# Kernel optimization log

Hardware: AMD Instinct MI355X
Metric: run time of the kernel (lower is better)

The kernel has to match this reference:

```python
import jax, jax.numpy as jnp
import numpy as np

N = 100000   # nodes
E = 1600000  # edges (avg degree 16)
D = 128      # input_dim == hidden_dim
H = 128
L = 3        # n_layers
G = 512      # num graphs in batch
LATENT = 64
BN_EPS = 1e-5
SLOPE = 0.2  # LeakyReLU negative slope


def setup_inputs() -> dict:
    key = jax.random.key(0)
    ks = jax.random.split(key, 12)
    s = 1.0 / np.sqrt(H)
    return {
        "x": jax.random.normal(ks[0], (N, D), jnp.float32),
        "edge_index": jax.random.randint(ks[1], (2, E), 0, N, dtype=jnp.int32),
        "batch": jnp.sort(jax.random.randint(ks[2], (N,), 0, G, dtype=jnp.int32)),
        "W1": jax.random.normal(ks[3], (L, D, H), jnp.float32) * s,
        "b1": jax.random.normal(ks[4], (L, H), jnp.float32) * 0.01,
        "g1": jnp.ones((L, H), jnp.float32),
        "beta1": jnp.zeros((L, H), jnp.float32),
        "rm1": jnp.zeros((L, H), jnp.float32),
        "rv1": jnp.ones((L, H), jnp.float32),
        "W2": jax.random.normal(ks[5], (L, H, H), jnp.float32) * s,
        "b2": jax.random.normal(ks[6], (L, H), jnp.float32) * 0.01,
        "bn_g": jnp.ones((H,), jnp.float32),
        "bn_b": jnp.zeros((H,), jnp.float32),
        "bn_rm": jnp.zeros((H,), jnp.float32),
        "bn_rv": jnp.ones((H,), jnp.float32),
        "fcW": jax.random.normal(ks[7], (H, LATENT), jnp.float32) * s,
        "fcb": jax.random.normal(ks[8], (LATENT,), jnp.float32) * 0.01,
    }


def _bn_eval(t, g, b, rm, rv):
    # BatchNorm1d in eval mode: normalize by running stats
    return g * (t - rm) * jax.lax.rsqrt(rv + BN_EPS) + b


def reference(x, edge_index, batch, W1, b1, g1, beta1, rm1, rv1, W2, b2,
              bn_g, bn_b, bn_rm, bn_rv, fcW, fcb):
    src, dst = edge_index[0], edge_index[1]
    h = x
    for i in range(L):
        # GINConv (eps=0): h_i <- MLP(h_i + sum_{j->i} h_j)
        agg = jax.ops.segment_sum(h[src], dst, num_segments=N)
        t = (h + agg) @ W1[i] + b1[i]
        t = jax.nn.leaky_relu(t, SLOPE)
        t = _bn_eval(t, g1[i], beta1[i], rm1[i], rv1[i])
        t = t @ W2[i] + b2[i]
        h = jax.nn.leaky_relu(t, SLOPE)
        # dropout: identity in eval mode
    # global add pool by graph id -> [G, H]
    pooled = jax.ops.segment_sum(h, batch, num_segments=G)
    pooled = _bn_eval(pooled, bn_g, bn_b, bn_rm, bn_rv)
    return pooled @ fcW + fcb
```

## Files before the change

kernel.cpp:

```cpp
#include <hip/hip_runtime.h>

#define NN 100000
#define EE 1600000
#define DD 128
#define HH 128
#define LL 3
#define GG 512
#define LATENT 64
#define BN_EPS 1e-5f
#define SLOPE 0.2f
#define NB_SCAN 391
#define ASTR 136

typedef __attribute__((ext_vector_type(8))) short short8;
typedef __attribute__((ext_vector_type(4))) float floatx4;

__device__ __forceinline__ float leaky(float t) { return t > 0.f ? t : SLOPE * t; }

__device__ __forceinline__ unsigned short f2bf(float x) {
    union { float f; unsigned int u; } v; v.f = x;
    unsigned int r = v.u + 0x7fffu + ((v.u >> 16) & 1u);
    return (unsigned short)(r >> 16);
}
__device__ __forceinline__ float bf_lo(unsigned int p) {
    union { unsigned int u; float f; } v; v.u = p << 16; return v.f;
}
__device__ __forceinline__ float bf_hi(unsigned int p) {
    union { unsigned int u; float f; } v; v.u = p & 0xffff0000u; return v.f;
}


__global__ void hist_kernel(const int* __restrict__ dst, int* __restrict__ deg, int* __restrict__ rank) {
    int e = blockIdx.x * blockDim.x + threadIdx.x;
    if (e < EE) rank[e] = atomicAdd(&deg[dst[e]], 1);
}

__global__ __launch_bounds__(256) void scan1(const int* __restrict__ deg, int* __restrict__ bsum) {
    __shared__ int lds[256];
    int n = blockIdx.x * 256 + threadIdx.x;
    lds[threadIdx.x] = (n < NN) ? deg[n] : 0;
    __syncthreads();
    for (int off = 128; off > 0; off >>= 1) {
        if (threadIdx.x < off) lds[threadIdx.x] += lds[threadIdx.x + off];
        __syncthreads();
    }
    if (threadIdx.x == 0) bsum[blockIdx.x] = lds[0];
}

__global__ __launch_bounds__(512) void scan2(int* bsum, int* row_ptr) {
    __shared__ int lds[512];
    int tid = threadIdx.x;
    int v = (tid < NB_SCAN) ? bsum[tid] : 0;
    lds[tid] = v;
    __syncthreads();
    for (int off = 1; off < 512; off <<= 1) {
        int t = (tid >= off) ? lds[tid - off] : 0;
        __syncthreads();
        lds[tid] += t;
        __syncthreads();
    }
    int inc = lds[tid];
    if (tid < NB_SCAN) bsum[tid] = inc - v;
    if (tid == NB_SCAN - 1) row_ptr[NN] = inc;
}

__global__ __launch_bounds__(256) void scan3(const int* __restrict__ deg, const int* __restrict__ bsumEx,
                                             int* __restrict__ row_ptr) {
    __shared__ int lds[256];
    int tid = threadIdx.x;
    int n = blockIdx.x * 256 + tid;
    int v = (n < NN) ? deg[n] : 0;
    lds[tid] = v;
    __syncthreads();
    for (int off = 1; off < 256; off <<= 1) {
        int t = (tid >= off) ? lds[tid - off] : 0;
        __syncthreads();
        lds[tid] += t;
        __syncthreads();
    }
    int ex = lds[tid] - v;
    if (n < NN) row_ptr[n] = bsumEx[blockIdx.x] + ex;
}

__global__ void fill2(const int* __restrict__ src, const int* __restrict__ dst,
                      const int* __restrict__ rank, const int* __restrict__ row_ptr,
                      int* __restrict__ col) {
    int e = blockIdx.x * blockDim.x + threadIdx.x;
    if (e < EE) col[row_ptr[dst[e]] + rank[e]] = src[e];
}

__global__ void gstart_kernel(const int* __restrict__ batch, int* __restrict__ gstart) {
    int n = blockIdx.x * blockDim.x + threadIdx.x;
    if (n >= NN) return;
    int b = batch[n];
    int pb = (n == 0) ? -1 : batch[n - 1];
    for (int g = pb + 1; g <= b; ++g) gstart[g] = n;
    if (n == NN - 1) {
        for (int g = b + 1; g <= GG; ++g) gstart[g] = NN;
    }
}


__global__ __launch_bounds__(256) void cvtX(const float2* __restrict__ x2, unsigned int* __restrict__ hx) {
    int i = blockIdx.x * 256 + threadIdx.x;
    if (i >= NN * 64) return;
    float2 v = x2[i];
    hx[i] = (unsigned int)f2bf(v.x) | ((unsigned int)f2bf(v.y) << 16);
}

__global__ __launch_bounds__(256) void cvtWall(const float* __restrict__ W1,
                                               const float* __restrict__ W2,
                                               uint4* __restrict__ Wf) {
    int t = blockIdx.x * 256 + threadIdx.x;
    if (t >= 6 * 2048) return;
    int mat = t >> 11;
    int idx = t & 2047;
    const float* W = ((mat & 1) ? W2 : W1) + (size_t)(mat >> 1) * 128 * 128;
    int lane = idx & 63;
    int tn = (idx >> 6) & 7;
    int kk = idx >> 9;
    int n = tn * 16 + (lane & 15);
    int kb = kk * 32 + (lane >> 4) * 8;
    unsigned int p[4];
#pragma unroll
    for (int jj = 0; jj < 4; ++jj) {
        unsigned short lo = f2bf(W[(kb + 2 * jj) * 128 + n]);
        unsigned short hi = f2bf(W[(kb + 2 * jj + 1) * 128 + n]);
        p[jj] = (unsigned int)lo | ((unsigned int)hi << 16);
    }
    Wf[t] = make_uint4(p[0], p[1], p[2], p[3]);
}

__global__ __launch_bounds__(256) void agg_bf16w8(const unsigned int* __restrict__ h,
                                                  const int* __restrict__ row_ptr,
                                                  const int* __restrict__ col,
                                                  unsigned int* __restrict__ u) {
    int node = blockIdx.x * 4 + (threadIdx.x >> 6);
    int lane = threadIdx.x & 63;
    if (node >= NN) return;
    const int grp = lane >> 3;
    const int sub = lane & 7;
    const uint4* hv = (const uint4*)h;

    float a[16] = {};
    if (grp == 0) {
        uint4 v0 = hv[(size_t)node * 16 + sub];
        uint4 v1 = hv[(size_t)node * 16 + 8 + sub];
        a[0] += bf_lo(v0.x); a[1] += bf_hi(v0.x);
        a[2] += bf_lo(v0.y); a[3] += bf_hi(v0.y);
        a[4] += bf_lo(v0.z); a[5] += bf_hi(v0.z);
        a[6] += bf_lo(v0.w); a[7] += bf_hi(v0.w);
        a[8] += bf_lo(v1.x); a[9] += bf_hi(v1.x);
        a[10] += bf_lo(v1.y); a[11] += bf_hi(v1.y);
        a[12] += bf_lo(v1.z); a[13] += bf_hi(v1.z);
        a[14] += bf_lo(v1.w); a[15] += bf_hi(v1.w);
    }
    int s = row_ptr[node], e = row_ptr[node + 1];
    for (int j = s + grp; j < e; j += 8) {
        int c = col[j];
        uint4 v0 = hv[(size_t)c * 16 + sub];
        uint4 v1 = hv[(size_t)c * 16 + 8 + sub];
        a[0] += bf_lo(v0.x); a[1] += bf_hi(v0.x);
        a[2] += bf_lo(v0.y); a[3] += bf_hi(v0.y);
        a[4] += bf_lo(v0.z); a[5] += bf_hi(v0.z);
        a[6] += bf_lo(v0.w); a[7] += bf_hi(v0.w);
        a[8] += bf_lo(v1.x); a[9] += bf_hi(v1.x);
        a[10] += bf_lo(v1.y); a[11] += bf_hi(v1.y);
        a[12] += bf_lo(v1.z); a[13] += bf_hi(v1.z);
        a[14] += bf_lo(v1.w); a[15] += bf_hi(v1.w);
    }
#pragma unroll
    for (int t = 0; t < 16; ++t) {
        a[t] += __shfl_xor(a[t], 8);
        a[t] += __shfl_xor(a[t], 16);
        a[t] += __shfl_xor(a[t], 32);
    }
    if (grp == 0) {
        uint4 o0, o1;
        o0.x = (unsigned int)f2bf(a[0]) | ((unsigned int)f2bf(a[1]) << 16);
        o0.y = (unsigned int)f2bf(a[2]) | ((unsigned int)f2bf(a[3]) << 16);
        o0.z = (unsigned int)f2bf(a[4]) | ((unsigned int)f2bf(a[5]) << 16);
        o0.w = (unsigned int)f2bf(a[6]) | ((unsigned int)f2bf(a[7]) << 16);
        o1.x = (unsigned int)f2bf(a[8]) | ((unsigned int)f2bf(a[9]) << 16);
        o1.y = (unsigned int)f2bf(a[10]) | ((unsigned int)f2bf(a[11]) << 16);
        o1.z = (unsigned int)f2bf(a[12]) | ((unsigned int)f2bf(a[13]) << 16);
        o1.w = (unsigned int)f2bf(a[14]) | ((unsigned int)f2bf(a[15]) << 16);
        ((uint4*)u)[(size_t)node * 16 + sub] = o0;
        ((uint4*)u)[(size_t)node * 16 + 8 + sub] = o1;
    }
}

__global__ __launch_bounds__(256) void mlp_fused(const unsigned short* __restrict__ A,
                                                 const uint4* __restrict__ W1f,
                                                 const uint4* __restrict__ W2f,
                                                 const float* __restrict__ b1,
                                                 const float* __restrict__ g,
                                                 const float* __restrict__ beta,
                                                 const float* __restrict__ rm,
                                                 const float* __restrict__ rv,
                                                 const float* __restrict__ b2,
                                                 unsigned short* __restrict__ Out) {
    __shared__ unsigned short aL[128 * ASTR];
    __shared__ unsigned short mL[4][32 * ASTR];
    const int tid = threadIdx.x;
    const int rb = blockIdx.x * 128;

    const uint4* Ag = (const uint4*)(A + (size_t)rb * 128);
#pragma unroll
    for (int it = 0; it < 8; ++it) {
        int idx = it * 256 + tid;
        int r = idx >> 4, c = idx & 15;
        uint4 v = make_uint4(0u, 0u, 0u, 0u);
        if (rb + r < NN) v = Ag[idx];
        *(uint4*)&aL[r * ASTR + c * 8] = v;
    }
    __syncthreads();

    const int wid = tid >> 6, lane = tid & 63;
    const int ml = lane & 15, q = lane >> 4;
    const int m0 = wid * 32;

    floatx4 acc[2][8] = {};
#pragma unroll
    for (int kk = 0; kk < 4; ++kk) {
        short8 af[2];
#pragma unroll
        for (int t = 0; t < 2; ++t)
            af[t] = *(const short8*)&aL[(m0 + t * 16 + ml) * ASTR + kk * 32 + q * 8];
#pragma unroll
        for (int tn = 0; tn < 8; ++tn) {
            uint4 bq = W1f[(kk * 8 + tn) * 64 + lane];
            short8 bf = *(short8*)&bq;
            acc[0][tn] = __builtin_amdgcn_mfma_f32_16x16x32_bf16(af[0], bf, acc[0][tn], 0, 0, 0);
            acc[1][tn] = __builtin_amdgcn_mfma_f32_16x16x32_bf16(af[1], bf, acc[1][tn], 0, 0, 0);
        }
    }

#pragma unroll
    for (int tn = 0; tn < 8; ++tn) {
        int c = tn * 16 + ml;
        float s = g[c] * rsqrtf(rv[c] + BN_EPS);
        float sh = beta[c] - s * rm[c];
        float bv = b1[c];
#pragma unroll
        for (int t = 0; t < 2; ++t)
#pragma unroll
            for (int r = 0; r < 4; ++r) {
                float val = leaky(acc[t][tn][r] + bv);
                val = s * val + sh;
                mL[wid][(t * 16 + q * 4 + r) * ASTR + c] = f2bf(val);
            }
    }
    __syncthreads();

    floatx4 acc2[2][8] = {};
#pragma unroll
    for (int kk = 0; kk < 4; ++kk) {
        short8 af[2];
#pragma unroll
        for (int t = 0; t < 2; ++t)
            af[t] = *(const short8*)&mL[wid][(t * 16 + ml) * ASTR + kk * 32 + q * 8];
#pragma unroll
        for (int tn = 0; tn < 8; ++tn) {
            uint4 bq = W2f[(kk * 8 + tn) * 64 + lane];
            short8 bf = *(short8*)&bq;
            acc2[0][tn] = __builtin_amdgcn_mfma_f32_16x16x32_bf16(af[0], bf, acc2[0][tn], 0, 0, 0);
            acc2[1][tn] = __builtin_amdgcn_mfma_f32_16x16x32_bf16(af[1], bf, acc2[1][tn], 0, 0, 0);
        }
    }

#pragma unroll
    for (int tn = 0; tn < 8; ++tn) {
        int c = tn * 16 + ml;
        float bv = b2[c];
#pragma unroll
        for (int t = 0; t < 2; ++t)
#pragma unroll
            for (int r = 0; r < 4; ++r) {
                int row = rb + m0 + t * 16 + q * 4 + r;
                if (row < NN)
                    Out[(size_t)row * 128 + c] = f2bf(leaky(acc2[t][tn][r] + bv));
            }
    }
}

__global__ __launch_bounds__(256) void pool_bf16(const unsigned int* __restrict__ h,
                                                 const int* __restrict__ gstart,
                                                 const float* __restrict__ bng,
                                                 const float* __restrict__ bnb,
                                                 const float* __restrict__ bnrm,
                                                 const float* __restrict__ bnrv,
                                                 float* __restrict__ pooled) {
    __shared__ float lds[4][128];
    int g = blockIdx.x;
    int wid = threadIdx.x >> 6, lane = threadIdx.x & 63;
    int s = gstart[g], e = gstart[g + 1];
    float ax = 0.f, ay = 0.f;
    for (int n = s + wid; n < e; n += 4) {
        unsigned int v = h[(size_t)n * 64 + lane];
        ax += bf_lo(v);
        ay += bf_hi(v);
    }
    lds[wid][lane * 2] = ax;
    lds[wid][lane * 2 + 1] = ay;
    __syncthreads();
    if (wid == 0) {
#pragma unroll
        for (int t = 0; t < 2; ++t) {
            int c = lane * 2 + t;
            float acc = lds[0][c] + lds[1][c] + lds[2][c] + lds[3][c];
            pooled[g * 128 + c] = bng[c] * (acc - bnrm[c]) * rsqrtf(bnrv[c] + BN_EPS) + bnb[c];
        }
    }
}

__global__ __launch_bounds__(64) void final_kernel(const float* __restrict__ pooled,
                                                   const float* __restrict__ fcW,
                                                   const float* __restrict__ fcb,
                                                   float* __restrict__ out) {
    int g = blockIdx.x;
    int l = threadIdx.x;
    float acc = fcb[l];
#pragma unroll 8
    for (int c = 0; c < HH; ++c) acc += pooled[g * 128 + c] * fcW[c * LATENT + l];
    out[g * LATENT + l] = acc;
}

extern "C" void kernel_launch(void* const* d_in, const int* in_sizes, int n_in,
                              void* d_out, int out_size, void* d_ws, size_t ws_size,
                              hipStream_t stream) {
    const float* x = (const float*)d_in[0];
    const int* ei = (const int*)d_in[1];
    const int* batch = (const int*)d_in[2];
    const float* W1 = (const float*)d_in[3];
    const float* b1 = (const float*)d_in[4];
    const float* g1 = (const float*)d_in[5];
    const float* beta1 = (const float*)d_in[6];
    const float* rm1 = (const float*)d_in[7];
    const float* rv1 = (const float*)d_in[8];
    const float* W2 = (const float*)d_in[9];
    const float* b2 = (const float*)d_in[10];
    const float* bn_g = (const float*)d_in[11];
    const float* bn_b = (const float*)d_in[12];
    const float* bn_rm = (const float*)d_in[13];
    const float* bn_rv = (const float*)d_in[14];
    const float* fcW = (const float*)d_in[15];
    const float* fcb = (const float*)d_in[16];
    float* out = (float*)d_out;

    const int* src = ei;
    const int* dst = ei + EE;

    char* w = (char*)d_ws;
    size_t off = 0;
    auto alloc = [&](size_t bytes) -> char* {
        char* p = w + off;
        off += (bytes + 1023) & ~(size_t)1023;
        return p;
    };
    unsigned int* hx = (unsigned int*)alloc(4 * (size_t)NN * 64);
    unsigned int* ubuf = (unsigned int*)alloc(4 * (size_t)NN * 64);
    unsigned int* hbuf = (unsigned int*)alloc(4 * (size_t)NN * 64);
    uint4* Wf = (uint4*)alloc(16 * (size_t)6 * 2048);
    int* deg = (int*)alloc(4 * (size_t)NN);
    int* row_ptr = (int*)alloc(4 * (size_t)(NN + 1));
    int* rank = (int*)alloc(4 * (size_t)EE);
    int* col = (int*)alloc(4 * (size_t)EE);
    int* bsum = (int*)alloc(4 * 512);
    int* gstart = (int*)alloc(4 * (GG + 1));
    float* pooled = (float*)alloc(sizeof(float) * GG * 128);
    (void)ws_size; (void)in_sizes; (void)n_in; (void)out_size;

    hipMemsetAsync(deg, 0, 4 * (size_t)NN, stream);
    hist_kernel<<<(EE + 255) / 256, 256, 0, stream>>>(dst, deg, rank);
    scan1<<<NB_SCAN, 256, 0, stream>>>(deg, bsum);
    scan2<<<1, 512, 0, stream>>>(bsum, row_ptr);
    scan3<<<NB_SCAN, 256, 0, stream>>>(deg, bsum, row_ptr);
    fill2<<<(EE + 255) / 256, 256, 0, stream>>>(src, dst, rank, row_ptr, col);
    gstart_kernel<<<(NN + 255) / 256, 256, 0, stream>>>(batch, gstart);

    cvtX<<<(NN * 64 + 255) / 256, 256, 0, stream>>>((const float2*)x, hx);
    cvtWall<<<48, 256, 0, stream>>>(W1, W2, Wf);

    const int gblocks = (NN + 127) / 128;
    const unsigned int* hcur = hx;
    for (int i = 0; i < LL; ++i) {
        agg_bf16w8<<<(NN + 3) / 4, 256, 0, stream>>>(hcur, row_ptr, col, ubuf);
        mlp_fused<<<gblocks, 256, 0, stream>>>((const unsigned short*)ubuf,
                                               Wf + (size_t)(2 * i) * 2048,
                                               Wf + (size_t)(2 * i + 1) * 2048,
                                               b1 + i * HH, g1 + i * HH, beta1 + i * HH,
                                               rm1 + i * HH, rv1 + i * HH, b2 + i * HH,
                                               (unsigned short*)hbuf);
        hcur = hbuf;
    }
    pool_bf16<<<GG, 256, 0, stream>>>(hbuf, gstart, bn_g, bn_b, bn_rm, bn_rv, pooled);
    final_kernel<<<GG, 64, 0, stream>>>(pooled, fcW, fcb, out);
}
```

Baseline: 563.2 us.

## Privatize degree histogram per XCD, merge prep kernels, pack aggregation into float2

The degree histogram now keeps a private copy per XCD, picked by reading the hardware XCC id, so atomics stay in each die's local L2 rather than bouncing across dies. A combine pass then computes per-XCD offsets, and fill writes CSR columns from those offsets. The gstart, weight-conversion and x-conversion kernels are merged into one launch to cut launch overhead. Aggregation accumulates in float2 vectors to allow packed adds. The cost is an 8x larger degree buffer plus its memset, and the code depends on reading an undocumented hardware register.

After: 564.6 us. Within noise of the previous version (+0.3%).

```diff
diff --git a/kernel.cpp b/kernel.cpp
--- a/kernel.cpp
+++ b/kernel.cpp
@@ -9,11 +9,13 @@
 #define LATENT 64
 #define BN_EPS 1e-5f
 #define SLOPE 0.2f
+#define ASTR 136
 #define NB_SCAN 391
-#define ASTR 136
+#define NXCD 8
 
 typedef __attribute__((ext_vector_type(8))) short short8;
 typedef __attribute__((ext_vector_type(4))) float floatx4;
+typedef __attribute__((ext_vector_type(2))) float floatx2;
 
 __device__ __forceinline__ float leaky(float t) { return t > 0.f ? t : SLOPE * t; }
 
@@ -28,17 +30,44 @@
 __device__ __forceinline__ float bf_hi(unsigned int p) {
     union { unsigned int u; float f; } v; v.u = p & 0xffff0000u; return v.f;
 }
-
-
-__global__ void hist_kernel(const int* __restrict__ dst, int* __restrict__ deg, int* __restrict__ rank) {
+__device__ __forceinline__ floatx2 up2(unsigned int p) {
+    union { unsigned int u; float f; } lo, hi;
+    lo.u = p << 16; hi.u = p & 0xffff0000u;
+    floatx2 r; r.x = lo.f; r.y = hi.f; return r;
+}
+
+__device__ __forceinline__ int xcc_id() {
+    int x;
+    asm volatile("s_getreg_b32 %0, hwreg(HW_REG_XCC_ID)" : "=s"(x));
+    return x & (NXCD - 1);
+}
+
+
+__global__ void hist_x(const int* __restrict__ dst, int* __restrict__ deg8, int* __restrict__ rank) {
+    int x = xcc_id();
     int e = blockIdx.x * blockDim.x + threadIdx.x;
-    if (e < EE) rank[e] = atomicAdd(&deg[dst[e]], 1);
-}
-
-__global__ __launch_bounds__(256) void scan1(const int* __restrict__ deg, int* __restrict__ bsum) {
+    if (e < EE) {
+        int d = dst[e];
+        int r = atomicAdd(&deg8[x * NN + d], 1);
+        rank[e] = (x << 24) | r;
+    }
+}
+
+__global__ __launch_bounds__(256) void combine(int* __restrict__ deg8, int* __restrict__ deg,
+                                               int* __restrict__ bsum) {
     __shared__ int lds[256];
     int n = blockIdx.x * 256 + threadIdx.x;
-    lds[threadIdx.x] = (n < NN) ? deg[n] : 0;
+    int tot = 0;
+    if (n < NN) {
+#pragma unroll
+        for (int x = 0; x < NXCD; ++x) {
+            int c = deg8[x * NN + n];
+            deg8[x * NN + n] = tot;
+            tot += c;
+        }
+        deg[n] = tot;
+    }
+    lds[threadIdx.x] = tot;
     __syncthreads();
     for (int off = 128; off > 0; off >>= 1) {
         if (threadIdx.x < off) lds[threadIdx.x] += lds[threadIdx.x + off];
@@ -82,54 +111,60 @@
     if (n < NN) row_ptr[n] = bsumEx[blockIdx.x] + ex;
 }
 
-__global__ void fill2(const int* __restrict__ src, const int* __restrict__ dst,
+__global__ void fill3(const int* __restrict__ src, const int* __restrict__ dst,
                       const int* __restrict__ rank, const int* __restrict__ row_ptr,
-                      int* __restrict__ col) {
+                      const int* __restrict__ xoff, int* __restrict__ col) {
     int e = blockIdx.x * blockDim.x + threadIdx.x;
-    if (e < EE) col[row_ptr[dst[e]] + rank[e]] = src[e];
-}
-
-__global__ void gstart_kernel(const int* __restrict__ batch, int* __restrict__ gstart) {
-    int n = blockIdx.x * blockDim.x + threadIdx.x;
-    if (n >= NN) return;
-    int b = batch[n];
-    int pb = (n == 0) ? -1 : batch[n - 1];
-    for (int g = pb + 1; g <= b; ++g) gstart[g] = n;
-    if (n == NN - 1) {
-        for (int g = b + 1; g <= GG; ++g) gstart[g] = NN;
-    }
-}
-
-
-__global__ __launch_bounds__(256) void cvtX(const float2* __restrict__ x2, unsigned int* __restrict__ hx) {
-    int i = blockIdx.x * 256 + threadIdx.x;
-    if (i >= NN * 64) return;
-    float2 v = x2[i];
-    hx[i] = (unsigned int)f2bf(v.x) | ((unsigned int)f2bf(v.y) << 16);
-}
-
-__global__ __launch_bounds__(256) void cvtWall(const float* __restrict__ W1,
-                                               const float* __restrict__ W2,
-                                               uint4* __restrict__ Wf) {
-    int t = blockIdx.x * 256 + threadIdx.x;
-    if (t >= 6 * 2048) return;
-    int mat = t >> 11;
-    int idx = t & 2047;
-    const float* W = ((mat & 1) ? W2 : W1) + (size_t)(mat >> 1) * 128 * 128;
-    int lane = idx & 63;
-    int tn = (idx >> 6) & 7;
-    int kk = idx >> 9;
-    int n = tn * 16 + (lane & 15);
-    int kb = kk * 32 + (lane >> 4) * 8;
-    unsigned int p[4];
-#pragma unroll
-    for (int jj = 0; jj < 4; ++jj) {
-        unsigned short lo = f2bf(W[(kb + 2 * jj) * 128 + n]);
-        unsigned short hi = f2bf(W[(kb + 2 * jj + 1) * 128 + n]);
-        p[jj] = (unsigned int)lo | ((unsigned int)hi << 16);
-    }
-    Wf[t] = make_uint4(p[0], p[1], p[2], p[3]);
-}
+    if (e < EE) {
+        int d = dst[e];
+        int rk = rank[e];
+        int x = rk >> 24;
+        int lr = rk & 0xffffff;
+        col[row_ptr[d] + xoff[x * NN + d] + lr] = src[e];
+    }
+}
+
+#define PREP_GS 391
+#define PREP_W  (PREP_GS + 48)
+__global__ __launch_bounds__(256) void prep_kernel(const int* __restrict__ batch, int* __restrict__ gstart,
+                                                   const float* __restrict__ W1, const float* __restrict__ W2,
+                                                   uint4* __restrict__ Wf,
+                                                   const float2* __restrict__ x2, unsigned int* __restrict__ hx) {
+    int b = blockIdx.x;
+    if (b < PREP_GS) {
+        int n = b * 256 + threadIdx.x;
+        if (n >= NN) return;
+        int bb = batch[n];
+        int pb = (n == 0) ? -1 : batch[n - 1];
+        for (int g = pb + 1; g <= bb; ++g) gstart[g] = n;
+        if (n == NN - 1)
+            for (int g = bb + 1; g <= GG; ++g) gstart[g] = NN;
+    } else if (b < PREP_W) {
+        int t = (b - PREP_GS) * 256 + threadIdx.x;
+        int mat = t >> 11;
+        int idx = t & 2047;
+        const float* W = ((mat & 1) ? W2 : W1) + (size_t)(mat >> 1) * 128 * 128;
+        int lane = idx & 63;
+        int tn = (idx >> 6) & 7;
+        int kk = idx >> 9;
+        int n = tn * 16 + (lane & 15);
+        int kb = kk * 32 + (lane >> 4) * 8;
+        unsigned int p[4];
+#pragma unroll
+        for (int jj = 0; jj < 4; ++jj) {
+            unsigned short lo = f2bf(W[(kb + 2 * jj) * 128 + n]);
+            unsigned short hi = f2bf(W[(kb + 2 * jj + 1) * 128 + n]);
+            p[jj] = (unsigned int)lo | ((unsigned int)hi << 16);
+        }
+        Wf[t] = make_uint4(p[0], p[1], p[2], p[3]);
+    } else {
+        int i = (b - PREP_W) * 256 + threadIdx.x;
+        if (i >= NN * 64) return;
+        float2 v = x2[i];
+        hx[i] = (unsigned int)f2bf(v.x) | ((unsigned int)f2bf(v.y) << 16);
+    }
+}
+#define PREP_BLOCKS (PREP_W + (NN * 64 + 255) / 256)
 
 __global__ __launch_bounds__(256) void agg_bf16w8(const unsigned int* __restrict__ h,
                                                   const int* __restrict__ row_ptr,
@@ -142,49 +177,43 @@
     const int sub = lane & 7;
     const uint4* hv = (const uint4*)h;
 
-    float a[16] = {};
+    floatx2 a[8];
+#pragma unroll
+    for (int t = 0; t < 8; ++t) { a[t].x = 0.f; a[t].y = 0.f; }
+
     if (grp == 0) {
         uint4 v0 = hv[(size_t)node * 16 + sub];
         uint4 v1 = hv[(size_t)node * 16 + 8 + sub];
-        a[0] += bf_lo(v0.x); a[1] += bf_hi(v0.x);
-        a[2] += bf_lo(v0.y); a[3] += bf_hi(v0.y);
-        a[4] += bf_lo(v0.z); a[5] += bf_hi(v0.z);
-        a[6] += bf_lo(v0.w); a[7] += bf_hi(v0.w);
-        a[8] += bf_lo(v1.x); a[9] += bf_hi(v1.x);
-        a[10] += bf_lo(v1.y); a[11] += bf_hi(v1.y);
-        a[12] += bf_lo(v1.z); a[13] += bf_hi(v1.z);
-        a[14] += bf_lo(v1.w); a[15] += bf_hi(v1.w);
+        a[0] += up2(v0.x); a[1] += up2(v0.y); a[2] += up2(v0.z); a[3] += up2(v0.w);
+        a[4] += up2(v1.x); a[5] += up2(v1.y); a[6] += up2(v1.z); a[7] += up2(v1.w);
     }
     int s = row_ptr[node], e = row_ptr[node + 1];
     for (int j = s + grp; j < e; j += 8) {
         int c = col[j];
         uint4 v0 = hv[(size_t)c * 16 + sub];
         uint4 v1 = hv[(size_t)c * 16 + 8 + sub];
-        a[0] += bf_lo(v0.x); a[1] += bf_hi(v0.x);
-        a[2] += bf_lo(v0.y); a[3] += bf_hi(v0.y);
-        a[4] += bf_lo(v0.z); a[5] += bf_hi(v0.z);
-        a[6] += bf_lo(v0.w); a[7] += bf_hi(v0.w);
-        a[8] += bf_lo(v1.x); a[9] += bf_hi(v1.x);
-        a[10] += bf_lo(v1.y); a[11] += bf_hi(v1.y);
-        a[12] += bf_lo(v1.z); a[13] += bf_hi(v1.z);
-        a[14] += bf_lo(v1.w); a[15] += bf_hi(v1.w);
-    }
-#pragma unroll
-    for (int t = 0; t < 16; ++t) {
-        a[t] += __shfl_xor(a[t], 8);
-        a[t] += __shfl_xor(a[t], 16);
-        a[t] += __shfl_xor(a[t], 32);
+        a[0] += up2(v0.x); a[1] += up2(v0.y); a[2] += up2(v0.z); a[3] += up2(v0.w);
+        a[4] += up2(v1.x); a[5] += up2(v1.y); a[6] += up2(v1.z); a[7] += up2(v1.w);
+    }
+#pragma unroll
+    for (int t = 0; t < 8; ++t) {
+        a[t].x += __shfl_xor(a[t].x, 8);
+        a[t].y += __shfl_xor(a[t].y, 8);
+        a[t].x += __shfl_xor(a[t].x, 16);
+        a[t].y += __shfl_xor(a[t].y, 16);
+        a[t].x += __shfl_xor(a[t].x, 32);
+        a[t].y += __shfl_xor(a[t].y, 32);
     }
     if (grp == 0) {
         uint4 o0, o1;
-        o0.x = (unsigned int)f2bf(a[0]) | ((unsigned int)f2bf(a[1]) << 16);
-        o0.y = (unsigned int)f2bf(a[2]) | ((unsigned int)f2bf(a[3]) << 16);
-        o0.z = (unsigned int)f2bf(a[4]) | ((unsigned int)f2bf(a[5]) << 16);
-        o0.w = (unsigned int)f2bf(a[6]) | ((unsigned int)f2bf(a[7]) << 16);
-        o1.x = (unsigned int)f2bf(a[8]) | ((unsigned int)f2bf(a[9]) << 16);
-        o1.y = (unsigned int)f2bf(a[10]) | ((unsigned int)f2bf(a[11]) << 16);
-        o1.z = (unsigned int)f2bf(a[12]) | ((unsigned int)f2bf(a[13]) << 16);
-        o1.w = (unsigned int)f2bf(a[14]) | ((unsigned int)f2bf(a[15]) << 16);
+        o0.x = (unsigned int)f2bf(a[0].x) | ((unsigned int)f2bf(a[0].y) << 16);
+        o0.y = (unsigned int)f2bf(a[1].x) | ((unsigned int)f2bf(a[1].y) << 16);
+        o0.z = (unsigned int)f2bf(a[2].x) | ((unsigned int)f2bf(a[2].y) << 16);
+        o0.w = (unsigned int)f2bf(a[3].x) | ((unsigned int)f2bf(a[3].y) << 16);
+        o1.x = (unsigned int)f2bf(a[4].x) | ((unsigned int)f2bf(a[4].y) << 16);
+        o1.y = (unsigned int)f2bf(a[5].x) | ((unsigned int)f2bf(a[5].y) << 16);
+        o1.z = (unsigned int)f2bf(a[6].x) | ((unsigned int)f2bf(a[6].y) << 16);
+        o1.w = (unsigned int)f2bf(a[7].x) | ((unsigned int)f2bf(a[7].y) << 16);
         ((uint4*)u)[(size_t)node * 16 + sub] = o0;
         ((uint4*)u)[(size_t)node * 16 + 8 + sub] = o1;
     }
@@ -362,6 +391,7 @@
     unsigned int* ubuf = (unsigned int*)alloc(4 * (size_t)NN * 64);
     unsigned int* hbuf = (unsigned int*)alloc(4 * (size_t)NN * 64);
     uint4* Wf = (uint4*)alloc(16 * (size_t)6 * 2048);
+    int* deg8 = (int*)alloc(4 * (size_t)NXCD * NN);
     int* deg = (int*)alloc(4 * (size_t)NN);
     int* row_ptr = (int*)alloc(4 * (size_t)(NN + 1));
     int* rank = (int*)alloc(4 * (size_t)EE);
@@ -371,16 +401,14 @@
     float* pooled = (float*)alloc(sizeof(float) * GG * 128);
     (void)ws_size; (void)in_sizes; (void)n_in; (void)out_size;
 
-    hipMemsetAsync(deg, 0, 4 * (size_t)NN, stream);
-    hist_kernel<<<(EE + 255) / 256, 256, 0, stream>>>(dst, deg, rank);
-    scan1<<<NB_SCAN, 256, 0, stream>>>(deg, bsum);
+    hipMemsetAsync(deg8, 0, 4 * (size_t)NXCD * NN, stream);
+    hist_x<<<(EE + 255) / 256, 256, 0, stream>>>(dst, deg8, rank);
+    combine<<<NB_SCAN, 256, 0, stream>>>(deg8, deg, bsum);
     scan2<<<1, 512, 0, stream>>>(bsum, row_ptr);
     scan3<<<NB_SCAN, 256, 0, stream>>>(deg, bsum, row_ptr);
-    fill2<<<(EE + 255) / 256, 256, 0, stream>>>(src, dst, rank, row_ptr, col);
-    gstart_kernel<<<(NN + 255) / 256, 256, 0, stream>>>(batch, gstart);
-
-    cvtX<<<(NN * 64 + 255) / 256, 256, 0, stream>>>((const float2*)x, hx);
-    cvtWall<<<48, 256, 0, stream>>>(W1, W2, Wf);
+    fill3<<<(EE + 255) / 256, 256, 0, stream>>>(src, dst, rank, row_ptr, deg8, col);
+
+    prep_kernel<<<PREP_BLOCKS, 256, 0, stream>>>(batch, gstart, W1, W2, Wf, (const float2*)x, hx);
 
     const int gblocks = (NN + 127) / 128;
     const unsigned int* hcur = hx;
```
